# Kernel optimization log

Measured on AMD Instinct MI355X. Metric: run time of the kernel, lower is better.

The kernel has to match this reference:

```python
import jax, jax.numpy as jnp
import numpy as np

B, N, D, H, C = 4, 1024, 768, 12, 3
Dh = D // H                      # 64
HID = int(D * 4.0 * (2.0 / 3.0)) # 2048 (SwiGLU hidden)
EPS = 1e-5


def layernorm(x, g, b):
    m = jnp.mean(x, axis=-1, keepdims=True)
    v = jnp.mean(jnp.square(x - m), axis=-1, keepdims=True)
    return (x - m) * jax.lax.rsqrt(v + EPS) * g + b


def setup_inputs() -> dict:
    key = jax.random.key(0)
    ks = jax.random.split(key, 8)
    x = jax.random.normal(ks[0], (B, N, D), jnp.float32)
    coords = jax.random.uniform(ks[1], (B, N, C), jnp.float32)
    qkv_w = jax.random.normal(ks[2], (3 * D, D), jnp.float32) * 0.02
    qkv_b = jnp.zeros((3 * D,), jnp.float32)
    rel_w = jax.random.normal(ks[3], (H, C), jnp.float32) * 0.1
    ln1_g = jnp.ones((D,), jnp.float32)
    ln1_b = jnp.zeros((D,), jnp.float32)
    ln2_g = jnp.ones((D,), jnp.float32)
    ln2_b = jnp.zeros((D,), jnp.float32)
    win_w = jax.random.normal(ks[4], (2 * HID, D), jnp.float32) * 0.02
    win_b = jnp.zeros((2 * HID,), jnp.float32)
    wout_w = jax.random.normal(ks[5], (D, HID), jnp.float32) * 0.02
    wout_b = jnp.zeros((D,), jnp.float32)
    return dict(x=x, coords=coords, ln1_g=ln1_g, ln1_b=ln1_b, qkv_w=qkv_w,
                qkv_b=qkv_b, rel_w=rel_w, ln2_g=ln2_g, ln2_b=ln2_b,
                win_w=win_w, win_b=win_b, wout_w=wout_w, wout_b=wout_b)


def reference(x, coords, ln1_g, ln1_b, qkv_w, qkv_b, rel_w, ln2_g, ln2_b,
              win_w, win_b, wout_w, wout_b):
    # --- PatchAttention on norm1(x) ---
    h = layernorm(x, ln1_g, ln1_b)
    qkv = h @ qkv_w.T + qkv_b                    # (B,N,3D)
    q, k, v = jnp.split(qkv, 3, axis=-1)

    def heads(t):  # (B,N,D) -> (B,H,N,Dh)
        return t.reshape(B, N, H, Dh).transpose(0, 2, 1, 3)

    qh, kh, vh = heads(q), heads(k), heads(v)
    scale = 1.0 / np.sqrt(Dh).astype(np.float32)
    scores = jnp.einsum('bhid,bhjd->bhij', qh, kh) * scale
    # coord bias: (coords_i - coords_j) . W_h  ==  p[b,h,i] - p[b,h,j]
    p = jnp.einsum('bnc,hc->bhn', coords, rel_w)  # (B,H,N)
    scores = scores + p[:, :, :, None] - p[:, :, None, :]
    attn = jax.nn.softmax(scores, axis=-1)
    o = jnp.einsum('bhij,bhjd->bhid', attn, vh)   # (B,H,N,Dh)
    o = o.transpose(0, 2, 1, 3).reshape(B, N, D)
    x = x + o

    # --- SwiGLU FFN on norm2(x) ---
    h2 = layernorm(x, ln2_g, ln2_b)
    uv = h2 @ win_w.T + win_b                     # (B,N,2*HID)
    u, g = jnp.split(uv, 2, axis=-1)
    act = jax.nn.silu(u) * g
    return x + act @ wout_w.T + wout_b
```

## Files before the change

kernel.cpp:

```cpp
#include <hip/hip_runtime.h>
#include <math.h>

typedef unsigned short u16;
typedef __bf16 bf16x8 __attribute__((ext_vector_type(8)));
typedef __bf16 bf16x4 __attribute__((ext_vector_type(4)));
typedef u16 u16x4 __attribute__((ext_vector_type(4)));
typedef float f32x4 __attribute__((ext_vector_type(4)));

#define NTOK 1024
#define DMODEL 768
#define NHEAD 12
#define LD3 2304
#define HIDDIM 2048

__device__ __forceinline__ float b2f(u16 u) {
  unsigned int t = ((unsigned int)u) << 16;
  float f;
  __builtin_memcpy(&f, &t, 4);
  return f;
}
__device__ __forceinline__ u16 f2b(float f) {
  unsigned int t;
  __builtin_memcpy(&t, &f, 4);
  t += 0x7fffu + ((t >> 16) & 1u);
  return (u16)(t >> 16);
}

__device__ __forceinline__ void gl_lds16(const u16* g, u16* l) {
  __builtin_amdgcn_global_load_lds(
      (__attribute__((address_space(1))) const unsigned int*)g,
      (__attribute__((address_space(3))) unsigned int*)l, 16, 0, 0);
}

__global__ __launch_bounds__(256) void signal_kernel(float* __restrict__ out,
                                                     int n, float c) {
  int i = blockIdx.x * 256 + threadIdx.x;
  if (i < n) out[i] = c;
}

__global__ __launch_bounds__(256) void detect_kernel(const u16* __restrict__ x,
                                                     int* __restrict__ flag) {
  __shared__ int cnt;
  if (threadIdx.x == 0) cnt = 0;
  __syncthreads();
  int bad = 0;
  for (int i = threadIdx.x; i < 4096; i += 256) {
    u16 v = x[2 * i];
    int e = (v >> 7) & 0xFF;
    if (e >= 0xC0) bad++;
  }
  atomicAdd(&cnt, bad);
  __syncthreads();
  if (threadIdx.x == 0) *flag = (cnt >= 64) ? 1 : 0;
}

struct CanonJobs {
  const void* s[13];
  u16* d[13];
  int n[13];
};

__global__ __launch_bounds__(256) void canon_kernel(CanonJobs jobs,
                                                    const int* __restrict__ flag) {
  int j = blockIdx.y;
  int n = jobs.n[j];
  const void* s = jobs.s[j];
  u16* d = jobs.d[j];
  bool isf32 = (*flag != 0);
  for (int i = blockIdx.x * 256 + threadIdx.x; i < n; i += gridDim.x * 256) {
    d[i] = isf32 ? f2b(((const float*)s)[i]) : ((const u16*)s)[i];
  }
}

__global__ __launch_bounds__(256) void ln_bf16_kernel(
    const u16* __restrict__ x, const u16* __restrict__ g,
    const u16* __restrict__ b, u16* __restrict__ out) {
  int row = blockIdx.x;
  int tid = threadIdx.x;
  const u16* xr = x + (size_t)row * DMODEL;
  float v0 = b2f(xr[tid]), v1 = b2f(xr[tid + 256]), v2 = b2f(xr[tid + 512]);
  float s = v0 + v1 + v2;
  float q = v0 * v0 + v1 * v1 + v2 * v2;
#pragma unroll
  for (int off = 32; off; off >>= 1) {
    s += __shfl_xor(s, off, 64);
    q += __shfl_xor(q, off, 64);
  }
  __shared__ float rs[4], rq[4];
  int wv = tid >> 6;
  if ((tid & 63) == 0) { rs[wv] = s; rq[wv] = q; }
  __syncthreads();
  s = rs[0] + rs[1] + rs[2] + rs[3];
  q = rq[0] + rq[1] + rq[2] + rq[3];
  float mean = s * (1.0f / 768.0f);
  float var = q * (1.0f / 768.0f) - mean * mean;
  float inv = rsqrtf(var + 1e-5f);
  u16* outr = out + (size_t)row * DMODEL;
  outr[tid]       = f2b((v0 - mean) * inv * b2f(g[tid])       + b2f(b[tid]));
  outr[tid + 256] = f2b((v1 - mean) * inv * b2f(g[tid + 256]) + b2f(b[tid + 256]));
  outr[tid + 512] = f2b((v2 - mean) * inv * b2f(g[tid + 512]) + b2f(b[tid + 512]));
}

__global__ __launch_bounds__(256) void ln_f32_kernel(
    const float* __restrict__ x, const u16* __restrict__ g,
    const u16* __restrict__ b, u16* __restrict__ out) {
  int row = blockIdx.x;
  int tid = threadIdx.x;
  const float* xr = x + (size_t)row * DMODEL;
  float v0 = xr[tid], v1 = xr[tid + 256], v2 = xr[tid + 512];
  float s = v0 + v1 + v2;
  float q = v0 * v0 + v1 * v1 + v2 * v2;
#pragma unroll
  for (int off = 32; off; off >>= 1) {
    s += __shfl_xor(s, off, 64);
    q += __shfl_xor(q, off, 64);
  }
  __shared__ float rs[4], rq[4];
  int wv = tid >> 6;
  if ((tid & 63) == 0) { rs[wv] = s; rq[wv] = q; }
  __syncthreads();
  s = rs[0] + rs[1] + rs[2] + rs[3];
  q = rq[0] + rq[1] + rq[2] + rq[3];
  float mean = s * (1.0f / 768.0f);
  float var = q * (1.0f / 768.0f) - mean * mean;
  float inv = rsqrtf(var + 1e-5f);
  u16* outr = out + (size_t)row * DMODEL;
  outr[tid]       = f2b((v0 - mean) * inv * b2f(g[tid])       + b2f(b[tid]));
  outr[tid + 256] = f2b((v1 - mean) * inv * b2f(g[tid + 256]) + b2f(b[tid + 256]));
  outr[tid + 512] = f2b((v2 - mean) * inv * b2f(g[tid + 512]) + b2f(b[tid + 512]));
}

__device__ __forceinline__ void gemm128_mainloop(
    const u16* __restrict__ A, const u16* __restrict__ W, int K,
    int mB0, int nB0, u16* Al, u16* Bl, f32x4 (&acc)[4][4]) {
  int lane = threadIdx.x & 63;
  int wv = threadIdx.x >> 6;
  int q16 = lane & 15, quad = lane >> 4;
  int mW = (wv >> 1) * 64, nW = (wv & 1) * 64;
  int srow = lane >> 2, scol = (lane & 3) * 8;
  for (int k0 = 0; k0 < K; k0 += 32) {
#pragma unroll
    for (int c = 0; c < 2; ++c) {
      int ch = wv * 2 + c;
      int r = ch * 16 + srow;
      gl_lds16(A + (size_t)(mB0 + r) * K + k0 + scol, Al + ch * 512);
      gl_lds16(W + (size_t)(nB0 + r) * K + k0 + scol, Bl + ch * 512);
    }
    __syncthreads();
    bf16x8 af[4], bfr[4];
#pragma unroll
    for (int si = 0; si < 4; ++si)
      af[si] = *(const bf16x8*)((const __bf16*)Al + (mW + si * 16 + q16) * 32 + quad * 8);
#pragma unroll
    for (int sj = 0; sj < 4; ++sj)
      bfr[sj] = *(const bf16x8*)((const __bf16*)Bl + (nW + sj * 16 + q16) * 32 + quad * 8);
#pragma unroll
    for (int si = 0; si < 4; ++si)
#pragma unroll
      for (int sj = 0; sj < 4; ++sj)
        acc[si][sj] = __builtin_amdgcn_mfma_f32_16x16x32_bf16(af[si], bfr[sj], acc[si][sj], 0, 0, 0);
    __syncthreads();
  }
}

__global__ __launch_bounds__(256) void gemm_bt(
    const u16* __restrict__ Ap, const u16* __restrict__ Wp,
    const u16* __restrict__ bias, u16* __restrict__ Cp, int Nn, int K) {
  __shared__ __align__(16) u16 Al[128 * 32], Bl[128 * 32];
  int lane = threadIdx.x & 63;
  int wv = threadIdx.x >> 6;
  int q16 = lane & 15, quad = lane >> 4;
  int mBase = blockIdx.y * 128 + (wv >> 1) * 64;
  int nBase = blockIdx.x * 128 + (wv & 1) * 64;
  f32x4 acc[4][4] = {};
  gemm128_mainloop(Ap, Wp, K, blockIdx.y * 128, blockIdx.x * 128, Al, Bl, acc);
#pragma unroll
  for (int si = 0; si < 4; ++si)
#pragma unroll
    for (int sj = 0; sj < 4; ++sj) {
      int col = nBase + sj * 16 + q16;
      float bcol = b2f(bias[col]);
#pragma unroll
      for (int r = 0; r < 4; ++r) {
        int rowi = mBase + si * 16 + quad * 4 + r;
        Cp[(size_t)rowi * Nn + col] = f2b(acc[si][sj][r] + bcol);
      }
    }
}

__global__ __launch_bounds__(256) void gemm_out_split(
    const u16* __restrict__ Ap, const u16* __restrict__ Wp,
    const u16* __restrict__ bias, const float* __restrict__ res,
    float* __restrict__ part, float* __restrict__ out) {
  __shared__ __align__(16) u16 Al[128 * 32], Bl[64 * 32];
  int lane = threadIdx.x & 63;
  int wv = threadIdx.x >> 6;
  int q16 = lane & 15, quad = lane >> 4;
  int mB0 = blockIdx.y * 128;
  int nB0 = blockIdx.x * 64;
  int kz = blockIdx.z;
  int kbase = kz * 1024;
  int mW = (wv >> 1) * 64, nW = (wv & 1) * 32;
  int srow = lane >> 2, scol = (lane & 3) * 8;
  f32x4 acc[4][2] = {};
  for (int k0 = 0; k0 < 1024; k0 += 32) {
#pragma unroll
    for (int c = 0; c < 2; ++c) {
      int ch = wv * 2 + c;
      int r = ch * 16 + srow;
      gl_lds16(Ap + (size_t)(mB0 + r) * 2048 + kbase + k0 + scol, Al + ch * 512);
    }
    {
      int r = wv * 16 + srow;
      gl_lds16(Wp + (size_t)(nB0 + r) * 2048 + kbase + k0 + scol, Bl + wv * 512);
    }
    __syncthreads();
    bf16x8 af[4], bfr[2];
#pragma unroll
    for (int si = 0; si < 4; ++si)
      af[si] = *(const bf16x8*)((const __bf16*)Al + (mW + si * 16 + q16) * 32 + quad * 8);
#pragma unroll
    for (int sj = 0; sj < 2; ++sj)
      bfr[sj] = *(const bf16x8*)((const __bf16*)Bl + (nW + sj * 16 + q16) * 32 + quad * 8);
#pragma unroll
    for (int si = 0; si < 4; ++si)
#pragma unroll
      for (int sj = 0; sj < 2; ++sj)
        acc[si][sj] = __builtin_amdgcn_mfma_f32_16x16x32_bf16(af[si], bfr[sj], acc[si][sj], 0, 0, 0);
    __syncthreads();
  }
#pragma unroll
  for (int si = 0; si < 4; ++si)
#pragma unroll
    for (int sj = 0; sj < 2; ++sj) {
      int col = nB0 + nW + sj * 16 + q16;
#pragma unroll
      for (int r = 0; r < 4; ++r) {
        int rowi = mB0 + mW + si * 16 + quad * 4 + r;
        size_t idx = (size_t)rowi * 768 + col;
        if (kz == 0) {
          part[idx] = acc[si][sj][r];
        } else {
          out[idx] = acc[si][sj][r] + b2f(bias[col]) + res[idx];
        }
      }
    }
}

__global__ __launch_bounds__(256) void add_kernel(float* __restrict__ out,
                                                  const float* __restrict__ part) {
  int i = blockIdx.x * 256 + threadIdx.x;
  f32x4 o = ((f32x4*)out)[i];
  f32x4 p = ((const f32x4*)part)[i];
#pragma unroll
  for (int r = 0; r < 4; ++r) o[r] += p[r];
  ((f32x4*)out)[i] = o;
}

__global__ __launch_bounds__(256) void ffn_in_kernel(
    const u16* __restrict__ hp, const u16* __restrict__ Wp,
    const u16* __restrict__ bias, u16* __restrict__ actp) {
  __shared__ __align__(16) u16 Al[128 * 32], Bl[128 * 32];
  int lane = threadIdx.x & 63;
  int wv = threadIdx.x >> 6;
  int q16 = lane & 15, quad = lane >> 4;
  int mB0 = blockIdx.y * 128;
  int cB0 = blockIdx.x * 64;
  int mW = (wv >> 1) * 64;
  int cW = (wv & 1) * 32;
  int srow = lane >> 2, scol = (lane & 3) * 8;
  f32x4 au[4][2] = {}, ag[4][2] = {};
  for (int k0 = 0; k0 < DMODEL; k0 += 32) {
#pragma unroll
    for (int c = 0; c < 2; ++c) {
      int ch = wv * 2 + c;
      int r = ch * 16 + srow;
      gl_lds16(hp + (size_t)(mB0 + r) * DMODEL + k0 + scol, Al + ch * 512);
      int grow = (r < 64) ? (cB0 + r) : (HIDDIM + cB0 + r - 64);
      gl_lds16(Wp + (size_t)grow * DMODEL + k0 + scol, Bl + ch * 512);
    }
    __syncthreads();
    bf16x8 af[4], wu[2], wg[2];
#pragma unroll
    for (int si = 0; si < 4; ++si)
      af[si] = *(const bf16x8*)((const __bf16*)Al + (mW + si * 16 + q16) * 32 + quad * 8);
#pragma unroll
    for (int sj = 0; sj < 2; ++sj) {
      wu[sj] = *(const bf16x8*)((const __bf16*)Bl + (cW + sj * 16 + q16) * 32 + quad * 8);
      wg[sj] = *(const bf16x8*)((const __bf16*)Bl + (64 + cW + sj * 16 + q16) * 32 + quad * 8);
    }
#pragma unroll
    for (int si = 0; si < 4; ++si)
#pragma unroll
      for (int sj = 0; sj < 2; ++sj) {
        au[si][sj] = __builtin_amdgcn_mfma_f32_16x16x32_bf16(af[si], wu[sj], au[si][sj], 0, 0, 0);
        ag[si][sj] = __builtin_amdgcn_mfma_f32_16x16x32_bf16(af[si], wg[sj], ag[si][sj], 0, 0, 0);
      }
    __syncthreads();
  }
#pragma unroll
  for (int si = 0; si < 4; ++si)
#pragma unroll
    for (int sj = 0; sj < 2; ++sj) {
      int col = cB0 + cW + sj * 16 + q16;
      float bu = b2f(bias[col]);
      float bg = b2f(bias[HIDDIM + col]);
#pragma unroll
      for (int r = 0; r < 4; ++r) {
        int rowi = mB0 + mW + si * 16 + quad * 4 + r;
        float u = au[si][sj][r] + bu;
        float g = ag[si][sj][r] + bg;
        float s = u / (1.0f + __expf(-u));
        actp[(size_t)rowi * HIDDIM + col] = f2b(s * g);
      }
    }
}

__global__ __launch_bounds__(256) void p_kernel(
    const u16* __restrict__ coords, const u16* __restrict__ relw,
    float* __restrict__ p) {
  const float LOG2E = 1.4426950408889634f;
  int idx = blockIdx.x * 256 + threadIdx.x;
  float c0 = b2f(coords[idx * 3 + 0]);
  float c1 = b2f(coords[idx * 3 + 1]);
  float c2 = b2f(coords[idx * 3 + 2]);
  int b = idx >> 10, n = idx & 1023;
#pragma unroll
  for (int h = 0; h < NHEAD; ++h) {
    float w0 = b2f(relw[h * 3 + 0]), w1 = b2f(relw[h * 3 + 1]), w2 = b2f(relw[h * 3 + 2]);
    p[(size_t)(b * NHEAD + h) * NTOK + n] = (c0 * w0 + c1 * w1 + c2 * w2) * LOG2E;
  }
}

__global__ __launch_bounds__(256) void vt_kernel(const u16* __restrict__ qkvp,
                                                 u16* __restrict__ vtp) {
  int blk = blockIdx.x;
  int b = blk / 192;
  int rem = blk % 192;
  int h = rem >> 4;
  int nt = rem & 15;
  int wv = threadIdx.x >> 6;
  int d = threadIdx.x & 63;
  int n0 = nt * 64 + wv * 16;
  const u16* src = qkvp + ((size_t)(b * NTOK) + n0) * LD3 + 2 * DMODEL + h * 64 + d;
  u16* dst = vtp + ((size_t)((b * NHEAD + h) * 64 + d)) * NTOK + n0;
#pragma unroll
  for (int c = 0; c < 2; ++c) {
    u16 buf[8] __attribute__((aligned(16)));
#pragma unroll
    for (int i = 0; i < 8; ++i) buf[i] = src[(size_t)(c * 8 + i) * LD3];
    *(uint4*)(dst + c * 8) = *(const uint4*)buf;
  }
}

__global__ __launch_bounds__(256) void attn_kernel(
    const u16* __restrict__ qkvp, const u16* __restrict__ vtp,
    const float* __restrict__ p2, const u16* __restrict__ xp,
    float* __restrict__ x1) {
  const __bf16* qb = (const __bf16*)qkvp;
  __shared__ __align__(16) u16 Kl[4][32 * 64];
  __shared__ __align__(16) u16 Vl[4][64 * 32];
  __shared__ __align__(16) u16 Pl[4][16][40];
  __shared__ __align__(16) float Pb[1024];
  int lane = threadIdx.x & 63;
  int wv = threadIdx.x >> 6;
  int hw = blockIdx.x;
  int g = hw % 48;
  int nt = hw / 48;
  int b = g / 12, h = g % 12;
  int i0 = (nt * 4 + wv) * 16;
  int q16 = lane & 15, quad = lane >> 4;

  const float scl2 = 0.125f * 1.4426950408889634f;

  const __bf16* qrow = qb + ((size_t)(b * NTOK) + i0 + q16) * LD3 + h * 64;
  bf16x8 bq0 = *(const bf16x8*)(qrow + quad * 8);
  bf16x8 bq1 = *(const bf16x8*)(qrow + 32 + quad * 8);

  const float* prow = p2 + (size_t)(b * NHEAD + h) * NTOK;

  int krw = wv * 8 + (lane >> 3);
  int ks  = (lane & 7) ^ (krw & 7);
  const u16* kg0 = qkvp + (size_t)(b * NTOK) * LD3 + DMODEL + h * 64 + ks * 8;
  int vrw = wv * 16 + (lane >> 2);
  int vs  = (lane & 3) ^ (vrw & 3);
  const u16* vg0 = vtp + ((size_t)((b * NHEAD + h) * 64 + vrw)) * NTOK + vs * 8;

  float mrun = -1e30f, lsum = 0.f;
  f32x4 accO[4] = {};

  gl_lds16((const u16*)(prow + wv * 256 + lane * 4), (u16*)&Pb[wv * 256]);
#pragma unroll
  for (int tt = 0; tt < 3; ++tt) {
    gl_lds16(kg0 + (size_t)(tt * 32 + krw) * LD3, &Kl[tt][wv * 512]);
    gl_lds16(vg0 + tt * 32, &Vl[tt][wv * 512]);
  }

  for (int t = 0; t < 32; ++t) {
    if (t < 30)       asm volatile("s_waitcnt vmcnt(4)" ::: "memory");
    else if (t == 30) asm volatile("s_waitcnt vmcnt(2)" ::: "memory");
    else              asm volatile("s_waitcnt vmcnt(0)" ::: "memory");
    __builtin_amdgcn_sched_barrier(0);
    __builtin_amdgcn_s_barrier();
    __builtin_amdgcn_sched_barrier(0);
    if (t < 29) {
      int j = (t + 3) * 32;
      gl_lds16(kg0 + (size_t)(j + krw) * LD3, &Kl[(t + 3) & 3][wv * 512]);
      gl_lds16(vg0 + j, &Vl[(t + 3) & 3][wv * 512]);
    }

    int j0 = t * 32;
    const __bf16* Kb = (const __bf16*)Kl[t & 3];
    int kx0 = (quad ^ (q16 & 7)) << 3;
    int kx1 = ((4 | quad) ^ (q16 & 7)) << 3;
    bf16x8 ka00 = *(const bf16x8*)(Kb + q16 * 64 + kx0);
    bf16x8 ka01 = *(const bf16x8*)(Kb + q16 * 64 + kx1);
    bf16x8 ka10 = *(const bf16x8*)(Kb + (16 + q16) * 64 + kx0);
    bf16x8 ka11 = *(const bf16x8*)(Kb + (16 + q16) * 64 + kx1);
    f32x4 st0 = {}, st1 = {};
    st0 = __builtin_amdgcn_mfma_f32_16x16x32_bf16(ka00, bq0, st0, 0, 0, 0);
    st0 = __builtin_amdgcn_mfma_f32_16x16x32_bf16(ka01, bq1, st0, 0, 0, 0);
    st1 = __builtin_amdgcn_mfma_f32_16x16x32_bf16(ka10, bq0, st1, 0, 0, 0);
    st1 = __builtin_amdgcn_mfma_f32_16x16x32_bf16(ka11, bq1, st1, 0, 0, 0);

    f32x4 pjl = *(const f32x4*)(&Pb[j0 + 4 * quad]);
    f32x4 pjh = *(const f32x4*)(&Pb[j0 + 16 + 4 * quad]);
    float sl[4], sh[4];
#pragma unroll
    for (int r = 0; r < 4; ++r) {
      sl[r] = st0[r] * scl2 - pjl[r];
      sh[r] = st1[r] * scl2 - pjh[r];
    }
    float lm = fmaxf(fmaxf(fmaxf(sl[0], sl[1]), fmaxf(sl[2], sl[3])),
                     fmaxf(fmaxf(sh[0], sh[1]), fmaxf(sh[2], sh[3])));
    lm = fmaxf(lm, __shfl_xor(lm, 16, 64));
    lm = fmaxf(lm, __shfl_xor(lm, 32, 64));
    float mn = fmaxf(mrun, lm);
    float alpha = exp2f(mrun - mn);
    mrun = mn;
    float pl[4], ph[4];
#pragma unroll
    for (int r = 0; r < 4; ++r) {
      pl[r] = exp2f(sl[r] - mn);
      ph[r] = exp2f(sh[r] - mn);
    }
    float ts = (pl[0] + pl[1]) + (pl[2] + pl[3]) +
               (ph[0] + ph[1]) + (ph[2] + ph[3]);
    ts += __shfl_xor(ts, 16, 64);
    ts += __shfl_xor(ts, 32, 64);
    lsum = lsum * alpha + ts;

    bf16x4 w0 = {(__bf16)pl[0], (__bf16)pl[1], (__bf16)pl[2], (__bf16)pl[3]};
    bf16x4 w1 = {(__bf16)ph[0], (__bf16)ph[1], (__bf16)ph[2], (__bf16)ph[3]};
    *(bf16x4*)(&Pl[wv][q16][4 * quad]) = w0;
    *(bf16x4*)(&Pl[wv][q16][16 + 4 * quad]) = w1;
    bf16x8 ap = *(const bf16x8*)(&Pl[wv][q16][quad * 8]);

    const __bf16* Vb = (const __bf16*)Vl[t & 3];
    int vx = (quad ^ (q16 & 3)) << 3;
#pragma unroll
    for (int ds = 0; ds < 4; ++ds) {
      bf16x8 av = *(const bf16x8*)(Vb + (ds * 16 + q16) * 32 + vx);
      f32x4 c = accO[ds];
#pragma unroll
      for (int r = 0; r < 4; ++r) c[r] *= alpha;
      accO[ds] = __builtin_amdgcn_mfma_f32_16x16x32_bf16(av, ap, c, 0, 0, 0);
    }
  }

  float rl = 1.0f / lsum;
  size_t rowbase = ((size_t)(b * NTOK) + i0 + q16) * DMODEL + h * 64;
#pragma unroll
  for (int ds = 0; ds < 4; ++ds) {
    int d0 = ds * 16 + quad * 4;
    u16x4 xv = *(const u16x4*)(xp + rowbase + d0);
    f32x4 ov;
#pragma unroll
    for (int r = 0; r < 4; ++r) ov[r] = b2f(xv[r]) + accO[ds][r] * rl;
    *(f32x4*)(x1 + rowbase + d0) = ov;
  }
}

extern "C" void kernel_launch(void* const* d_in, const int* in_sizes, int n_in,
                              void* d_out, int out_size, void* d_ws, size_t ws_size,
                              hipStream_t stream) {
  static const int esz[13] = {3145728, 12288, 768, 768, 1769472, 2304, 36,
                              768, 768, 3145728, 4096, 1572864, 768};
  float sig = -1.f;
  if (n_in != 13) {
    sig = 6000.f + 100.f * (float)n_in;
  } else {
    for (int i = 0; i < 13; ++i)
      if (in_sizes[i] != esz[i]) { sig = 1000.f + 100.f * (float)i; break; }
  }
  if (sig < 0.f && ws_size < 57258496ULL) sig = 3000.f;
  if (sig < 0.f && out_size != 3145728) sig = 3100.f;
  if (sig >= 0.f) {
    signal_kernel<<<(out_size + 255) / 256, 256, 0, stream>>>((float*)d_out, out_size, sig);
    return;
  }

  char* ws = (char*)d_ws;
  int*  flag    = (int*)ws;
  u16*  cx      = (u16*)(ws + 256);
  u16*  cqkvw   = (u16*)(ws + 6291712);
  u16*  cwinw   = (u16*)(ws + 9830656);
  u16*  cwoutw  = (u16*)(ws + 16122112);
  u16*  ccoords = (u16*)(ws + 19267840);
  u16*  cln1g   = (u16*)(ws + 19292416);
  u16*  cln1b   = (u16*)(ws + 19293952);
  u16*  cqkvb   = (u16*)(ws + 19295488);
  u16*  crelw   = (u16*)(ws + 19300096);
  u16*  cln2g   = (u16*)(ws + 19300352);
  u16*  cln2b   = (u16*)(ws + 19301888);
  u16*  cwinb   = (u16*)(ws + 19303424);
  u16*  cwoutb  = (u16*)(ws + 19311616);
  u16*  h       = (u16*)(ws + 19313152);
  u16*  qkv     = (u16*)(ws + 25604608);
  float* pbuf   = (float*)(ws + 44478976);
  float* x1     = (float*)(ws + 44675584);
  u16*  act     = qkv;
  u16*  vt      = h;
  float* part   = (float*)(ws + 256);

  detect_kernel<<<1, 256, 0, stream>>>((const u16*)d_in[0], flag);

  CanonJobs jobs;
  u16* dsts[13] = {cx, ccoords, cln1g, cln1b, cqkvw, cqkvb, crelw,
                   cln2g, cln2b, cwinw, cwinb, cwoutw, cwoutb};
  for (int i = 0; i < 13; ++i) {
    jobs.s[i] = d_in[i];
    jobs.d[i] = dsts[i];
    jobs.n[i] = in_sizes[i];
  }
  canon_kernel<<<dim3(3072, 13), 256, 0, stream>>>(jobs, flag);

  ln_bf16_kernel<<<4096, 256, 0, stream>>>(cx, cln1g, cln1b, h);
  gemm_bt<<<dim3(18, 32), 256, 0, stream>>>(h, cqkvw, cqkvb, qkv, 2304, 768);
  p_kernel<<<16, 256, 0, stream>>>(ccoords, crelw, pbuf);
  vt_kernel<<<768, 256, 0, stream>>>(qkv, vt);
  attn_kernel<<<768, 256, 0, stream>>>(qkv, vt, pbuf, cx, x1);
  ln_f32_kernel<<<4096, 256, 0, stream>>>(x1, cln2g, cln2b, h);
  ffn_in_kernel<<<dim3(32, 32), 256, 0, stream>>>(h, cwinw, cwinb, act);
  gemm_out_split<<<dim3(12, 32, 2), 256, 0, stream>>>(act, cwoutw, cwoutb, x1,
                                                      part, (float*)d_out);
  add_kernel<<<3072, 256, 0, stream>>>((float*)d_out, part);
}
```

Measured before the change: 289.2 us.

## Triple-buffer LDS tiles in GEMM kernels with two-stage prefetch

Converts the QKV/generic GEMM, FFN-in and FFN-out split-K main loops from a load-sync-compute-sync pattern to a three-slot LDS ring. Global-to-LDS loads run two k-steps ahead, with explicit vmcnt waits and a single barrier per step. The goal is to hide global memory latency behind MFMA work and drop one barrier per iteration. In exchange it triples LDS use per block, which may lower occupancy, and it depends on hand-counted vmcnt values being correct.

Measured after the change: 290.8 us. Within noise of the previous version (+0.6%).

```diff
diff --git a/kernel.cpp b/kernel.cpp
--- a/kernel.cpp
+++ b/kernel.cpp
@@ -130,7 +130,7 @@
   outr[tid + 512] = f2b((v2 - mean) * inv * b2f(g[tid + 512]) + b2f(b[tid + 512]));
 }
 
-__device__ __forceinline__ void gemm128_mainloop(
+__device__ __forceinline__ void gemm128_pipe(
     const u16* __restrict__ A, const u16* __restrict__ W, int K,
     int mB0, int nB0, u16* Al, u16* Bl, f32x4 (&acc)[4][4]) {
   int lane = threadIdx.x & 63;
@@ -138,42 +138,63 @@
   int q16 = lane & 15, quad = lane >> 4;
   int mW = (wv >> 1) * 64, nW = (wv & 1) * 64;
   int srow = lane >> 2, scol = (lane & 3) * 8;
-  for (int k0 = 0; k0 < K; k0 += 32) {
-#pragma unroll
-    for (int c = 0; c < 2; ++c) {
-      int ch = wv * 2 + c;
-      int r = ch * 16 + srow;
-      gl_lds16(A + (size_t)(mB0 + r) * K + k0 + scol, Al + ch * 512);
-      gl_lds16(W + (size_t)(nB0 + r) * K + k0 + scol, Bl + ch * 512);
-    }
-    __syncthreads();
+  int r0 = wv * 32 + srow, r1 = r0 + 16;
+  const u16* Ag0 = A + (size_t)(mB0 + r0) * K + scol;
+  const u16* Ag1 = A + (size_t)(mB0 + r1) * K + scol;
+  const u16* Wg0 = W + (size_t)(nB0 + r0) * K + scol;
+  const u16* Wg1 = W + (size_t)(nB0 + r1) * K + scol;
+  int ch0 = wv * 1024, ch1 = ch0 + 512;
+  int nsteps = K >> 5;
+#pragma unroll
+  for (int tt = 0; tt < 2; ++tt) {
+    int k0 = tt * 32;
+    gl_lds16(Ag0 + k0, Al + tt * 4096 + ch0);
+    gl_lds16(Wg0 + k0, Bl + tt * 4096 + ch0);
+    gl_lds16(Ag1 + k0, Al + tt * 4096 + ch1);
+    gl_lds16(Wg1 + k0, Bl + tt * 4096 + ch1);
+  }
+  for (int t = 0; t < nsteps; ++t) {
+    if (t < nsteps - 1) asm volatile("s_waitcnt vmcnt(4)" ::: "memory");
+    else                asm volatile("s_waitcnt vmcnt(0)" ::: "memory");
+    __builtin_amdgcn_sched_barrier(0);
+    __builtin_amdgcn_s_barrier();
+    __builtin_amdgcn_sched_barrier(0);
+    if (t < nsteps - 2) {
+      int k0 = (t + 2) * 32;
+      int bs = ((t + 2) % 3) * 4096;
+      gl_lds16(Ag0 + k0, Al + bs + ch0);
+      gl_lds16(Wg0 + k0, Bl + bs + ch0);
+      gl_lds16(Ag1 + k0, Al + bs + ch1);
+      gl_lds16(Wg1 + k0, Bl + bs + ch1);
+    }
+    const __bf16* Ab = (const __bf16*)(Al + (t % 3) * 4096);
+    const __bf16* Bb = (const __bf16*)(Bl + (t % 3) * 4096);
     bf16x8 af[4], bfr[4];
 #pragma unroll
     for (int si = 0; si < 4; ++si)
-      af[si] = *(const bf16x8*)((const __bf16*)Al + (mW + si * 16 + q16) * 32 + quad * 8);
+      af[si] = *(const bf16x8*)(Ab + (mW + si * 16 + q16) * 32 + quad * 8);
 #pragma unroll
     for (int sj = 0; sj < 4; ++sj)
-      bfr[sj] = *(const bf16x8*)((const __bf16*)Bl + (nW + sj * 16 + q16) * 32 + quad * 8);
+      bfr[sj] = *(const bf16x8*)(Bb + (nW + sj * 16 + q16) * 32 + quad * 8);
 #pragma unroll
     for (int si = 0; si < 4; ++si)
 #pragma unroll
       for (int sj = 0; sj < 4; ++sj)
         acc[si][sj] = __builtin_amdgcn_mfma_f32_16x16x32_bf16(af[si], bfr[sj], acc[si][sj], 0, 0, 0);
-    __syncthreads();
   }
 }
 
 __global__ __launch_bounds__(256) void gemm_bt(
     const u16* __restrict__ Ap, const u16* __restrict__ Wp,
     const u16* __restrict__ bias, u16* __restrict__ Cp, int Nn, int K) {
-  __shared__ __align__(16) u16 Al[128 * 32], Bl[128 * 32];
+  __shared__ __align__(16) u16 Al[3 * 128 * 32], Bl[3 * 128 * 32];
   int lane = threadIdx.x & 63;
   int wv = threadIdx.x >> 6;
   int q16 = lane & 15, quad = lane >> 4;
   int mBase = blockIdx.y * 128 + (wv >> 1) * 64;
   int nBase = blockIdx.x * 128 + (wv & 1) * 64;
   f32x4 acc[4][4] = {};
-  gemm128_mainloop(Ap, Wp, K, blockIdx.y * 128, blockIdx.x * 128, Al, Bl, acc);
+  gemm128_pipe(Ap, Wp, K, blockIdx.y * 128, blockIdx.x * 128, Al, Bl, acc);
 #pragma unroll
   for (int si = 0; si < 4; ++si)
 #pragma unroll
@@ -192,7 +213,7 @@
     const u16* __restrict__ Ap, const u16* __restrict__ Wp,
     const u16* __restrict__ bias, const float* __restrict__ res,
     float* __restrict__ part, float* __restrict__ out) {
-  __shared__ __align__(16) u16 Al[128 * 32], Bl[64 * 32];
+  __shared__ __align__(16) u16 Al[3 * 128 * 32], Bl[3 * 64 * 32];
   int lane = threadIdx.x & 63;
   int wv = threadIdx.x >> 6;
   int q16 = lane & 15, quad = lane >> 4;
@@ -202,32 +223,47 @@
   int kbase = kz * 1024;
   int mW = (wv >> 1) * 64, nW = (wv & 1) * 32;
   int srow = lane >> 2, scol = (lane & 3) * 8;
+  int r0 = wv * 32 + srow, r1 = r0 + 16;
+  int rb = wv * 16 + srow;
+  const u16* Ag0 = Ap + (size_t)(mB0 + r0) * 2048 + kbase + scol;
+  const u16* Ag1 = Ap + (size_t)(mB0 + r1) * 2048 + kbase + scol;
+  const u16* Wg  = Wp + (size_t)(nB0 + rb) * 2048 + kbase + scol;
+  int ch0 = wv * 1024, ch1 = ch0 + 512, chb = wv * 512;
   f32x4 acc[4][2] = {};
-  for (int k0 = 0; k0 < 1024; k0 += 32) {
-#pragma unroll
-    for (int c = 0; c < 2; ++c) {
-      int ch = wv * 2 + c;
-      int r = ch * 16 + srow;
-      gl_lds16(Ap + (size_t)(mB0 + r) * 2048 + kbase + k0 + scol, Al + ch * 512);
-    }
-    {
-      int r = wv * 16 + srow;
-      gl_lds16(Wp + (size_t)(nB0 + r) * 2048 + kbase + k0 + scol, Bl + wv * 512);
-    }
-    __syncthreads();
+#pragma unroll
+  for (int tt = 0; tt < 2; ++tt) {
+    int k0 = tt * 32;
+    gl_lds16(Ag0 + k0, Al + tt * 4096 + ch0);
+    gl_lds16(Ag1 + k0, Al + tt * 4096 + ch1);
+    gl_lds16(Wg + k0, Bl + tt * 2048 + chb);
+  }
+  for (int t = 0; t < 32; ++t) {
+    if (t < 31) asm volatile("s_waitcnt vmcnt(3)" ::: "memory");
+    else        asm volatile("s_waitcnt vmcnt(0)" ::: "memory");
+    __builtin_amdgcn_sched_barrier(0);
+    __builtin_amdgcn_s_barrier();
+    __builtin_amdgcn_sched_barrier(0);
+    if (t < 30) {
+      int k0 = (t + 2) * 32;
+      int bs = (t + 2) % 3;
+      gl_lds16(Ag0 + k0, Al + bs * 4096 + ch0);
+      gl_lds16(Ag1 + k0, Al + bs * 4096 + ch1);
+      gl_lds16(Wg + k0, Bl + bs * 2048 + chb);
+    }
+    const __bf16* Ab = (const __bf16*)(Al + (t % 3) * 4096);
+    const __bf16* Bb = (const __bf16*)(Bl + (t % 3) * 2048);
     bf16x8 af[4], bfr[2];
 #pragma unroll
     for (int si = 0; si < 4; ++si)
-      af[si] = *(const bf16x8*)((const __bf16*)Al + (mW + si * 16 + q16) * 32 + quad * 8);
+      af[si] = *(const bf16x8*)(Ab + (mW + si * 16 + q16) * 32 + quad * 8);
 #pragma unroll
     for (int sj = 0; sj < 2; ++sj)
-      bfr[sj] = *(const bf16x8*)((const __bf16*)Bl + (nW + sj * 16 + q16) * 32 + quad * 8);
+      bfr[sj] = *(const bf16x8*)(Bb + (nW + sj * 16 + q16) * 32 + quad * 8);
 #pragma unroll
     for (int si = 0; si < 4; ++si)
 #pragma unroll
       for (int sj = 0; sj < 2; ++sj)
         acc[si][sj] = __builtin_amdgcn_mfma_f32_16x16x32_bf16(af[si], bfr[sj], acc[si][sj], 0, 0, 0);
-    __syncthreads();
   }
 #pragma unroll
   for (int si = 0; si < 4; ++si)
@@ -260,7 +296,7 @@
 __global__ __launch_bounds__(256) void ffn_in_kernel(
     const u16* __restrict__ hp, const u16* __restrict__ Wp,
     const u16* __restrict__ bias, u16* __restrict__ actp) {
-  __shared__ __align__(16) u16 Al[128 * 32], Bl[128 * 32];
+  __shared__ __align__(16) u16 Al[3 * 128 * 32], Bl[3 * 128 * 32];
   int lane = threadIdx.x & 63;
   int wv = threadIdx.x >> 6;
   int q16 = lane & 15, quad = lane >> 4;
@@ -269,25 +305,47 @@
   int mW = (wv >> 1) * 64;
   int cW = (wv & 1) * 32;
   int srow = lane >> 2, scol = (lane & 3) * 8;
+  int r0 = wv * 32 + srow, r1 = r0 + 16;
+  int g0 = (r0 < 64) ? (cB0 + r0) : (HIDDIM + cB0 + r0 - 64);
+  int g1 = (r1 < 64) ? (cB0 + r1) : (HIDDIM + cB0 + r1 - 64);
+  const u16* Ag0 = hp + (size_t)(mB0 + r0) * DMODEL + scol;
+  const u16* Ag1 = hp + (size_t)(mB0 + r1) * DMODEL + scol;
+  const u16* Wg0 = Wp + (size_t)g0 * DMODEL + scol;
+  const u16* Wg1 = Wp + (size_t)g1 * DMODEL + scol;
+  int ch0 = wv * 1024, ch1 = ch0 + 512;
   f32x4 au[4][2] = {}, ag[4][2] = {};
-  for (int k0 = 0; k0 < DMODEL; k0 += 32) {
-#pragma unroll
-    for (int c = 0; c < 2; ++c) {
-      int ch = wv * 2 + c;
-      int r = ch * 16 + srow;
-      gl_lds16(hp + (size_t)(mB0 + r) * DMODEL + k0 + scol, Al + ch * 512);
-      int grow = (r < 64) ? (cB0 + r) : (HIDDIM + cB0 + r - 64);
-      gl_lds16(Wp + (size_t)grow * DMODEL + k0 + scol, Bl + ch * 512);
-    }
-    __syncthreads();
+#pragma unroll
+  for (int tt = 0; tt < 2; ++tt) {
+    int k0 = tt * 32;
+    gl_lds16(Ag0 + k0, Al + tt * 4096 + ch0);
+    gl_lds16(Wg0 + k0, Bl + tt * 4096 + ch0);
+    gl_lds16(Ag1 + k0, Al + tt * 4096 + ch1);
+    gl_lds16(Wg1 + k0, Bl + tt * 4096 + ch1);
+  }
+  for (int t = 0; t < 24; ++t) {
+    if (t < 23) asm volatile("s_waitcnt vmcnt(4)" ::: "memory");
+    else        asm volatile("s_waitcnt vmcnt(0)" ::: "memory");
+    __builtin_amdgcn_sched_barrier(0);
+    __builtin_amdgcn_s_barrier();
+    __builtin_amdgcn_sched_barrier(0);
+    if (t < 22) {
+      int k0 = (t + 2) * 32;
+      int bs = ((t + 2) % 3) * 4096;
+      gl_lds16(Ag0 + k0, Al + bs + ch0);
+      gl_lds16(Wg0 + k0, Bl + bs + ch0);
+      gl_lds16(Ag1 + k0, Al + bs + ch1);
+      gl_lds16(Wg1 + k0, Bl + bs + ch1);
+    }
+    const __bf16* Ab = (const __bf16*)(Al + (t % 3) * 4096);
+    const __bf16* Bb = (const __bf16*)(Bl + (t % 3) * 4096);
     bf16x8 af[4], wu[2], wg[2];
 #pragma unroll
     for (int si = 0; si < 4; ++si)
-      af[si] = *(const bf16x8*)((const __bf16*)Al + (mW + si * 16 + q16) * 32 + quad * 8);
+      af[si] = *(const bf16x8*)(Ab + (mW + si * 16 + q16) * 32 + quad * 8);
 #pragma unroll
     for (int sj = 0; sj < 2; ++sj) {
-      wu[sj] = *(const bf16x8*)((const __bf16*)Bl + (cW + sj * 16 + q16) * 32 + quad * 8);
-      wg[sj] = *(const bf16x8*)((const __bf16*)Bl + (64 + cW + sj * 16 + q16) * 32 + quad * 8);
+      wu[sj] = *(const bf16x8*)(Bb + (cW + sj * 16 + q16) * 32 + quad * 8);
+      wg[sj] = *(const bf16x8*)(Bb + (64 + cW + sj * 16 + q16) * 32 + quad * 8);
     }
 #pragma unroll
     for (int si = 0; si < 4; ++si)
@@ -296,7 +354,6 @@
         au[si][sj] = __builtin_amdgcn_mfma_f32_16x16x32_bf16(af[si], wu[sj], au[si][sj], 0, 0, 0);
         ag[si][sj] = __builtin_amdgcn_mfma_f32_16x16x32_bf16(af[si], wg[sj], ag[si][sj], 0, 0, 0);
       }
-    __syncthreads();
   }
 #pragma unroll
   for (int si = 0; si < 4; ++si)
```
